# Optimization experiments

Measured on AMD Instinct MI355X. Metric: run time of the kernel, lower is better.

## Reference

```python
import jax, jax.numpy as jnp
import numpy as np

H = 32

def setup_inputs() -> dict:
    key = jax.random.key(0)
    ks = jax.random.split(key, 8)
    B, S = 256, 4096
    scale = 1.0 / np.sqrt(H)
    return {
        "lstm_outputs": jax.random.normal(ks[0], (B, S, H), dtype=jnp.float32),
        "final_hidden": jax.random.normal(ks[1], (B, H), dtype=jnp.float32),
        "Wq": jax.random.uniform(ks[2], (H, H), jnp.float32, -scale, scale),
        "bq": jax.random.uniform(ks[3], (H,), jnp.float32, -scale, scale),
        "Wk": jax.random.uniform(ks[4], (H, H), jnp.float32, -scale, scale),
        "bk": jax.random.uniform(ks[5], (H,), jnp.float32, -scale, scale),
        "Wv": jax.random.uniform(ks[6], (H, 1), jnp.float32, -scale, scale),
        "bv": jax.random.uniform(ks[7], (1,), jnp.float32, -scale, scale),
    }

def reference(lstm_outputs, final_hidden, Wq, bq, Wk, bk, Wv, bv):
    # keys: [B,S,H], query: [B,H]
    keys = jnp.einsum('bsh,hd->bsd', lstm_outputs, Wk) + bk
    query = final_hidden @ Wq + bq
    tanhed = jnp.tanh(query[:, None, :] + keys)            # [B,S,H]
    scores = jnp.einsum('bsh,h->bs', tanhed, Wv[:, 0]) + bv[0]  # [B,S]
    att_weights = jax.nn.softmax(scores, axis=-1)          # [B,S]
    context = jnp.einsum('bs,bsh->bh', att_weights, keys)  # [B,H]
    return context, att_weights
```

## Files before the change

kernel.cpp:

```cpp
#include <hip/hip_runtime.h>
#include <math.h>

#define HD 32
#define BB 256
#define SS 4096
#define BLK 256
#define POSB 256
#define NCH (SS / POSB)
#define PAD 33
#define PART_STRIDE 33

__device__ __forceinline__ float tanh_fast(float x) {
  float e = __builtin_amdgcn_exp2f(x * 2.8853900817779268f);
  return 1.0f - 2.0f * __builtin_amdgcn_rcpf(e + 1.0f);
}
__device__ __forceinline__ float exp_fast(float x) {
  return __builtin_amdgcn_exp2f(x * 1.4426950408889634f);
}

__global__ void __launch_bounds__(BLK) bahdanau_p1(
    const float* __restrict__ lstm, const float* __restrict__ fh,
    const float* __restrict__ Wq, const float* __restrict__ bq,
    const float* __restrict__ Wk, const float* __restrict__ bk,
    const float* __restrict__ Wv, const float* __restrict__ bv,
    float* __restrict__ scores_out, float* __restrict__ partials) {
  __shared__ float sX[POSB * PAD];
  __shared__ float sE[POSB];
  __shared__ float sQ[HD];
  __shared__ float sRed[8][HD];
  __shared__ float sRedL[BLK / 64];

  const int tid = threadIdx.x;
  const int b = blockIdx.x / NCH;
  const int chunk = blockIdx.x % NCH;
  const int base = chunk * POSB;
  const int lane = tid & 63, wid = tid >> 6;

  const float* gx = lstm + ((size_t)b * SS + base) * HD;
  float4 stg[8];
#pragma unroll
  for (int i = 0; i < 8; i++) stg[i] = ((const float4*)gx)[tid + i * BLK];

  if (tid < HD) {
    float acc = bq[tid];
    const float* fhb = fh + b * HD;
#pragma unroll
    for (int j = 0; j < HD; j++) acc += fhb[j] * Wq[j * HD + tid];
    sQ[tid] = acc;
  }

#pragma unroll
  for (int i = 0; i < 8; i++) {
    const int f = tid + i * BLK;
    const int pos = f >> 3, q = f & 7;
    float* d = &sX[pos * PAD + q * 4];
    d[0] = stg[i].x; d[1] = stg[i].y; d[2] = stg[i].z; d[3] = stg[i].w;
  }
  __syncthreads();

  const float* xr = &sX[tid * PAD];
  float k[HD];
#pragma unroll
  for (int h = 0; h < HD; h++) k[h] = bk[h];
#pragma unroll
  for (int j = 0; j < HD; j++) {
    const float xj = xr[j];
#pragma unroll
    for (int h = 0; h < HD; h++) k[h] = fmaf(xj, Wk[j * HD + h], k[h]);
  }

  const float bv0 = bv[0];
  float sc = bv0;
#pragma unroll
  for (int h = 0; h < HD; h++)
    sc = fmaf(tanh_fast(sQ[h] + k[h]), Wv[h], sc);
  const float e = exp_fast(sc);
  scores_out[(size_t)b * SS + base + tid] = e;
  sE[tid] = e;

  float lv = e;
#pragma unroll
  for (int off = 32; off >= 1; off >>= 1) lv += __shfl_xor(lv, off, 64);
  if (lane == 0) sRedL[wid] = lv;

  float* kr = &sX[tid * PAD];
#pragma unroll
  for (int h = 0; h < HD; h++) kr[h] = k[h];
  __syncthreads();

  const int h = tid & 31, g = tid >> 5;
  float cp = 0.f;
#pragma unroll
  for (int p = 0; p < 32; p++) {
    const int pos = g * 32 + p;
    cp = fmaf(sE[pos], sX[pos * PAD + h], cp);
  }
  sRed[g][h] = cp;
  __syncthreads();

  if (tid < HD) {
    float c = 0.f;
#pragma unroll
    for (int gg = 0; gg < 8; gg++) c += sRed[gg][tid];
    float* p = partials + (size_t)blockIdx.x * PART_STRIDE;
    p[1 + tid] = c;
    if (tid == 0) p[0] = sRedL[0] + sRedL[1] + sRedL[2] + sRedL[3];
  }
}

__global__ void __launch_bounds__(BLK) bahdanau_p2(
    const float* __restrict__ partials, float* __restrict__ ctx_out,
    float* __restrict__ scores) {
  const int blk = blockIdx.x;
  const int b = blk >> 2;
  const int tid = threadIdx.x;

  float L = 0.f;
#pragma unroll
  for (int c = 0; c < NCH; c++)
    L += partials[(size_t)(b * NCH + c) * PART_STRIDE];
  const float invL = __builtin_amdgcn_rcpf(L);

  if ((blk & 3) == 0 && tid < HD) {
    float c = 0.f;
#pragma unroll
    for (int cc = 0; cc < NCH; cc++)
      c += partials[(size_t)(b * NCH + cc) * PART_STRIDE + 1 + tid];
    ctx_out[b * HD + tid] = c * invL;
  }

  float4* srow = (float4*)(scores + (size_t)b * SS + (blk & 3) * 1024);
  float4 s = srow[tid];
  s.x *= invL; s.y *= invL; s.z *= invL; s.w *= invL;
  srow[tid] = s;
}

extern "C" void kernel_launch(void* const* d_in, const int* in_sizes, int n_in,
                              void* d_out, int out_size, void* d_ws,
                              size_t ws_size, hipStream_t stream) {
  const float* lstm = (const float*)d_in[0];
  const float* fh   = (const float*)d_in[1];
  const float* Wq   = (const float*)d_in[2];
  const float* bq   = (const float*)d_in[3];
  const float* Wk   = (const float*)d_in[4];
  const float* bk   = (const float*)d_in[5];
  const float* Wv   = (const float*)d_in[6];
  const float* bv   = (const float*)d_in[7];

  float* out = (float*)d_out;
  float* ctx_out = out;
  float* scores = out + BB * HD;
  float* partials = (float*)d_ws;

  bahdanau_p1<<<BB * NCH, BLK, 0, stream>>>(lstm, fh, Wq, bq, Wk, bk, Wv, bv,
                                            scores, partials);
  bahdanau_p2<<<BB * 4, BLK, 0, stream>>>(partials, ctx_out, scores);
}
```

Measured before the change: 215.5 us.

## Apply Wk after the softmax reduction and stage Wk in shared memory

```diff
diff --git a/kernel.cpp b/kernel.cpp
--- a/kernel.cpp
+++ b/kernel.cpp
@@ -8,7 +8,7 @@
 #define POSB 256
 #define NCH (SS / POSB)
 #define PAD 33
-#define PART_STRIDE 33
+#define PSTRIDE 33
 
 __device__ __forceinline__ float tanh_fast(float x) {
   float e = __builtin_amdgcn_exp2f(x * 2.8853900817779268f);
@@ -18,23 +18,27 @@
   return __builtin_amdgcn_exp2f(x * 1.4426950408889634f);
 }
 
-__global__ void __launch_bounds__(BLK) bahdanau_p1(
+__global__ void __launch_bounds__(BLK, 4) bahdanau_p1(
     const float* __restrict__ lstm, const float* __restrict__ fh,
     const float* __restrict__ Wq, const float* __restrict__ bq,
     const float* __restrict__ Wk, const float* __restrict__ bk,
     const float* __restrict__ Wv, const float* __restrict__ bv,
     float* __restrict__ scores_out, float* __restrict__ partials) {
   __shared__ float sX[POSB * PAD];
+  __shared__ float sWk[HD * HD];
   __shared__ float sE[POSB];
-  __shared__ float sQ[HD];
-  __shared__ float sRed[8][HD];
+  __shared__ float sQB[HD];
+  __shared__ float sWv[HD];
+  __shared__ float sYp[8][HD];
   __shared__ float sRedL[BLK / 64];
 
   const int tid = threadIdx.x;
-  const int b = blockIdx.x / NCH;
-  const int chunk = blockIdx.x % NCH;
+  const int b = blockIdx.x >> 4;
+  const int chunk = blockIdx.x & (NCH - 1);
   const int base = chunk * POSB;
   const int lane = tid & 63, wid = tid >> 6;
+
+  ((float4*)sWk)[tid] = ((const float4*)Wk)[tid];
 
   const float* gx = lstm + ((size_t)b * SS + base) * HD;
   float4 stg[8];
@@ -42,11 +46,12 @@
   for (int i = 0; i < 8; i++) stg[i] = ((const float4*)gx)[tid + i * BLK];
 
   if (tid < HD) {
-    float acc = bq[tid];
+    float acc = bq[tid] + bk[tid];
     const float* fhb = fh + b * HD;
 #pragma unroll
     for (int j = 0; j < HD; j++) acc += fhb[j] * Wq[j * HD + tid];
-    sQ[tid] = acc;
+    sQB[tid] = acc;
+    sWv[tid] = Wv[tid];
   }
 
 #pragma unroll
@@ -59,21 +64,33 @@
   __syncthreads();
 
   const float* xr = &sX[tid * PAD];
-  float k[HD];
+  float acc[HD];
 #pragma unroll
-  for (int h = 0; h < HD; h++) k[h] = bk[h];
-#pragma unroll
+  for (int h = 0; h < HD; h++) acc[h] = 0.f;
+#pragma unroll 2
   for (int j = 0; j < HD; j++) {
     const float xj = xr[j];
+    const float4* wrow = (const float4*)&sWk[j * HD];
 #pragma unroll
-    for (int h = 0; h < HD; h++) k[h] = fmaf(xj, Wk[j * HD + h], k[h]);
+    for (int h4 = 0; h4 < 8; h4++) {
+      const float4 w = wrow[h4];
+      acc[4 * h4 + 0] = fmaf(xj, w.x, acc[4 * h4 + 0]);
+      acc[4 * h4 + 1] = fmaf(xj, w.y, acc[4 * h4 + 1]);
+      acc[4 * h4 + 2] = fmaf(xj, w.z, acc[4 * h4 + 2]);
+      acc[4 * h4 + 3] = fmaf(xj, w.w, acc[4 * h4 + 3]);
+    }
   }
 
-  const float bv0 = bv[0];
-  float sc = bv0;
+  float sc = bv[0];
 #pragma unroll
-  for (int h = 0; h < HD; h++)
-    sc = fmaf(tanh_fast(sQ[h] + k[h]), Wv[h], sc);
+  for (int h4 = 0; h4 < 8; h4++) {
+    const float4 qb = ((const float4*)sQB)[h4];
+    const float4 wv = ((const float4*)sWv)[h4];
+    sc = fmaf(tanh_fast(qb.x + acc[4 * h4 + 0]), wv.x, sc);
+    sc = fmaf(tanh_fast(qb.y + acc[4 * h4 + 1]), wv.y, sc);
+    sc = fmaf(tanh_fast(qb.z + acc[4 * h4 + 2]), wv.z, sc);
+    sc = fmaf(tanh_fast(qb.w + acc[4 * h4 + 3]), wv.w, sc);
+  }
   const float e = exp_fast(sc);
   scores_out[(size_t)b * SS + base + tid] = e;
   sE[tid] = e;
@@ -82,51 +99,58 @@
 #pragma unroll
   for (int off = 32; off >= 1; off >>= 1) lv += __shfl_xor(lv, off, 64);
   if (lane == 0) sRedL[wid] = lv;
-
-  float* kr = &sX[tid * PAD];
-#pragma unroll
-  for (int h = 0; h < HD; h++) kr[h] = k[h];
   __syncthreads();
 
-  const int h = tid & 31, g = tid >> 5;
+  const int j = tid & 31, g = tid >> 5;
   float cp = 0.f;
 #pragma unroll
   for (int p = 0; p < 32; p++) {
     const int pos = g * 32 + p;
-    cp = fmaf(sE[pos], sX[pos * PAD + h], cp);
+    cp = fmaf(sE[pos], sX[pos * PAD + j], cp);
   }
-  sRed[g][h] = cp;
+  sYp[g][j] = cp;
   __syncthreads();
 
   if (tid < HD) {
-    float c = 0.f;
+    float y = 0.f;
 #pragma unroll
-    for (int gg = 0; gg < 8; gg++) c += sRed[gg][tid];
-    float* p = partials + (size_t)blockIdx.x * PART_STRIDE;
-    p[1 + tid] = c;
+    for (int gg = 0; gg < 8; gg++) y += sYp[gg][tid];
+    float* p = partials + (size_t)blockIdx.x * PSTRIDE;
+    p[1 + tid] = y;
     if (tid == 0) p[0] = sRedL[0] + sRedL[1] + sRedL[2] + sRedL[3];
   }
 }
 
 __global__ void __launch_bounds__(BLK) bahdanau_p2(
-    const float* __restrict__ partials, float* __restrict__ ctx_out,
+    const float* __restrict__ partials, const float* __restrict__ Wk,
+    const float* __restrict__ bk, float* __restrict__ ctx_out,
     float* __restrict__ scores) {
   const int blk = blockIdx.x;
   const int b = blk >> 2;
   const int tid = threadIdx.x;
+  __shared__ float sY[HD];
 
   float L = 0.f;
 #pragma unroll
   for (int c = 0; c < NCH; c++)
-    L += partials[(size_t)(b * NCH + c) * PART_STRIDE];
+    L += partials[(size_t)(b * NCH + c) * PSTRIDE];
   const float invL = __builtin_amdgcn_rcpf(L);
 
-  if ((blk & 3) == 0 && tid < HD) {
-    float c = 0.f;
+  if ((blk & 3) == 0) {
+    if (tid < HD) {
+      float y = 0.f;
 #pragma unroll
-    for (int cc = 0; cc < NCH; cc++)
-      c += partials[(size_t)(b * NCH + cc) * PART_STRIDE + 1 + tid];
-    ctx_out[b * HD + tid] = c * invL;
+      for (int c = 0; c < NCH; c++)
+        y += partials[(size_t)(b * NCH + c) * PSTRIDE + 1 + tid];
+      sY[tid] = y;
+    }
+    __syncthreads();
+    if (tid < HD) {
+      float c = bk[tid] * L;
+#pragma unroll
+      for (int j = 0; j < HD; j++) c = fmaf(sY[j], Wk[j * HD + tid], c);
+      ctx_out[b * HD + tid] = c * invL;
+    }
   }
 
   float4* srow = (float4*)(scores + (size_t)b * SS + (blk & 3) * 1024);
@@ -154,5 +178,5 @@
 
   bahdanau_p1<<<BB * NCH, BLK, 0, stream>>>(lstm, fh, Wq, bq, Wk, bk, Wv, bv,
                                             scores, partials);
-  bahdanau_p2<<<BB * 4, BLK, 0, stream>>>(partials, ctx_out, scores);
+  bahdanau_p2<<<BB * 4, BLK, 0, stream>>>(partials, Wk, bk, ctx_out, scores);
 }
```

Measured after the change: 210.4 us. -2.3%, faster.
